# Kernel optimization log

Hardware: AMD Instinct MI355X
Metric: run time of the kernel (lower is better)

The kernel has to match this reference:

```python
import jax, jax.numpy as jnp
import numpy as np

B = 512
D = 64   # input feature dim
K = 63   # bilinear output dim (64 after the ones column)


def setup_inputs() -> dict:
    key = jax.random.key(0)
    ks = jax.random.split(key, 9)
    s = 1.0 / np.sqrt(D)  # torch Bilinear init scale (uniform bound); normal*s is fine for a baseline
    return {
        "x": jax.random.normal(ks[0], (B, D), jnp.float32),
        "y": jax.random.normal(ks[1], (B, D), jnp.float32),
        "z": jax.random.normal(ks[2], (B, D), jnp.float32),
        "W1": jax.random.normal(ks[3], (K, D, D), jnp.float32) * s,
        "b1": jax.random.normal(ks[4], (K,), jnp.float32) * s,
        "W2": jax.random.normal(ks[5], (K, D, D), jnp.float32) * s,
        "b2": jax.random.normal(ks[6], (K,), jnp.float32) * s,
        "W3": jax.random.normal(ks[7], (K, D, D), jnp.float32) * s,
        "b3": jax.random.normal(ks[8], (K,), jnp.float32) * s,
    }


def _bilinear(a, b, W, bias):
    # torch.nn.Bilinear: out[b,k] = sum_ij a[b,i] * W[k,i,j] * b[b,j] + bias[k]
    return jnp.einsum("bi,kij,bj->bk", a, W, b) + bias


def _append_ones(o):
    ones = jnp.ones((o.shape[0], 1), dtype=o.dtype)
    return jnp.concatenate([o, ones], axis=1)  # [B, 64]


def reference(x, y, z, W1, b1, W2, b2, W3, b3):
    o1 = _append_ones(_bilinear(x, y, W1, b1))  # [B,64]
    o2 = _append_ones(_bilinear(x, z, W2, b2))  # [B,64]
    o3 = _append_ones(_bilinear(y, z, W3, b3))  # [B,64]
    # bmm(o1[:,:,None], o2[:,None,:]).flatten then outer with o3 again:
    # index ordering is ((i*64 + j)*64 + k), matching bijk reshape.
    o123 = jnp.einsum("bi,bj,bk->bijk", o1, o2, o3)
    return o123.reshape(o123.shape[0], -1)  # [B, 262144]
```

## Files before the change

### kernel.cpp

```cpp
#include <hip/hip_runtime.h>
#include <hip/hip_bf16.h>

#define BATCH 512
#define DIM 64
#define KOUT 63

typedef float vf4 __attribute__((ext_vector_type(4)));

__global__ __launch_bounds__(256) void bilinear_kernel(
    const float* __restrict__ x, const float* __restrict__ y, const float* __restrict__ z,
    const float* __restrict__ W1, const float* __restrict__ b1,
    const float* __restrict__ W2, const float* __restrict__ b2,
    const float* __restrict__ W3, const float* __restrict__ b3,
    float* __restrict__ o ) {
    const int which = blockIdx.x >> 6;
    const int k     = blockIdx.x & 63;
    const int b     = blockIdx.y * 256 + threadIdx.x;

    float* outp = o + which * (BATCH * DIM);

    if (k == KOUT) {
        outp[b * DIM + KOUT] = 1.0f;
        return;
    }

    const float* A  = (which == 2) ? y : x;
    const float* C  = (which == 0) ? y : z;
    const float* W  = ((which == 0) ? W1 : (which == 1) ? W2 : W3) + k * (DIM * DIM);
    const float  bias = ((which == 0) ? b1 : (which == 1) ? b2 : b3)[k];

    __shared__ float sW[DIM * DIM];
    {
        const float4* W4  = (const float4*)W;
        float4*       sW4 = (float4*)sW;
        #pragma unroll
        for (int t = threadIdx.x; t < DIM * DIM / 4; t += 256) sW4[t] = W4[t];
    }
    __syncthreads();

    float c[DIM];
    {
        const float4* C4 = (const float4*)(C + b * DIM);
        #pragma unroll
        for (int q = 0; q < DIM / 4; q++) {
            float4 v = C4[q];
            c[4 * q + 0] = v.x; c[4 * q + 1] = v.y; c[4 * q + 2] = v.z; c[4 * q + 3] = v.w;
        }
    }

    const float* arow = A + b * DIM;
    const float4* sW4 = (const float4*)sW;
    float acc = bias;
    #pragma unroll 4
    for (int i = 0; i < DIM; i++) {
        float t = 0.0f;
        #pragma unroll
        for (int q = 0; q < DIM / 4; q++) {
            float4 w = sW4[i * (DIM / 4) + q];
            t = fmaf(w.x, c[4 * q + 0], t);
            t = fmaf(w.y, c[4 * q + 1], t);
            t = fmaf(w.z, c[4 * q + 2], t);
            t = fmaf(w.w, c[4 * q + 3], t);
        }
        acc = fmaf(arow[i], t, acc);
    }
    outp[b * DIM + k] = acc;
}

__global__ __launch_bounds__(256) void outer_kernel(
    const float* __restrict__ o , float* __restrict__ out) {
    const int b = blockIdx.x;
    __shared__ float s1[DIM];
    __shared__ float s2[DIM];
    __shared__ float s3f[DIM];

    const int t = threadIdx.x;
    if (t < 64)        s1[t]        = o[b * DIM + t];
    else if (t < 128)  s2[t - 64]   = o[BATCH * DIM + b * DIM + (t - 64)];
    else if (t < 192)  s3f[t - 128] = o[2 * BATCH * DIM + b * DIM + (t - 128)];
    __syncthreads();

    const vf4* s3 = (const vf4*)s3f;
    vf4* out4 = (vf4*)out + (size_t)b * 65536;

    #pragma unroll 4
    for (int f4 = t; f4 < 65536; f4 += 256) {
        const int k4 = f4 & 15;
        const int j  = (f4 >> 4) & 63;
        const int i  = f4 >> 10;
        const float s = s1[i] * s2[j];
        vf4 v = s3[k4] * s;
        __builtin_nontemporal_store(v, &out4[f4]);
    }
}

extern "C" void kernel_launch(void* const* d_in, const int* in_sizes, int n_in,
                              void* d_out, int out_size, void* d_ws, size_t ws_size,
                              hipStream_t stream) {
    const float* x  = (const float*)d_in[0];
    const float* y  = (const float*)d_in[1];
    const float* z  = (const float*)d_in[2];
    const float* W1 = (const float*)d_in[3];
    const float* b1 = (const float*)d_in[4];
    const float* W2 = (const float*)d_in[5];
    const float* b2 = (const float*)d_in[6];
    const float* W3 = (const float*)d_in[7];
    const float* b3 = (const float*)d_in[8];
    float* out = (float*)d_out;
    float* o   = (float*)d_ws;

    bilinear_kernel<<<dim3(192, 2), 256, 0, stream>>>(x, y, z, W1, b1, W2, b2, W3, b3, o);
    outer_kernel<<<dim3(BATCH), 256, 0, stream>>>(o, out);
}
```

Before: 568.3 us.

## Split outer-product kernel across 16 segments per batch row with precomputed scales

The outer kernel now launches 16 blocks per batch row, each writing a 4096-vector slice (four i values), instead of one block writing all 65536 vectors. Each thread precomputes its 16 s1*s2 products in registers and issues 16 fully unrolled nontemporal stores with no per-iteration index arithmetic or shared-memory reads. This raises the number of blocks in flight for the store-bound phase and removes the address and LDS work. In exchange, each block redundantly reloads the s2 and s3 rows, and every block pays its own launch and sync overhead.

```diff
diff --git a/kernel.cpp b/kernel.cpp
--- a/kernel.cpp
+++ b/kernel.cpp
@@ -1,5 +1,4 @@
 #include <hip/hip_runtime.h>
-#include <hip/hip_bf16.h>
 
 #define BATCH 512
 #define DIM 64
@@ -69,28 +68,35 @@
 
 __global__ __launch_bounds__(256) void outer_kernel(
     const float* __restrict__ o , float* __restrict__ out) {
-    const int b = blockIdx.x;
-    __shared__ float s1[DIM];
+    const int b   = blockIdx.x;
+    const int seg = blockIdx.y;
+
+    __shared__ float s1[4];
     __shared__ float s2[DIM];
     __shared__ float s3f[DIM];
 
     const int t = threadIdx.x;
-    if (t < 64)        s1[t]        = o[b * DIM + t];
-    else if (t < 128)  s2[t - 64]   = o[BATCH * DIM + b * DIM + (t - 64)];
-    else if (t < 192)  s3f[t - 128] = o[2 * BATCH * DIM + b * DIM + (t - 128)];
+    if (t < 64)        s2[t]        = o[BATCH * DIM + b * DIM + t];
+    else if (t < 128)  s3f[t - 64]  = o[2 * BATCH * DIM + b * DIM + (t - 64)];
+    else if (t < 132)  s1[t - 128]  = o[b * DIM + seg * 4 + (t - 128)];
     __syncthreads();
 
-    const vf4* s3 = (const vf4*)s3f;
-    vf4* out4 = (vf4*)out + (size_t)b * 65536;
+    const vf4 v3 = ((const vf4*)s3f)[t & 15];
+    const int jb = t >> 4;
 
-    #pragma unroll 4
-    for (int f4 = t; f4 < 65536; f4 += 256) {
-        const int k4 = f4 & 15;
-        const int j  = (f4 >> 4) & 63;
-        const int i  = f4 >> 10;
-        const float s = s1[i] * s2[j];
-        vf4 v = s3[k4] * s;
-        __builtin_nontemporal_store(v, &out4[f4]);
+    float p[4][4];
+    #pragma unroll
+    for (int ii = 0; ii < 4; ++ii) {
+        const float a = s1[ii];
+        #pragma unroll
+        for (int jc = 0; jc < 4; ++jc) p[ii][jc] = a * s2[jb + 16 * jc];
+    }
+
+    vf4* out4 = (vf4*)out + (size_t)b * 65536 + seg * 4096 + t;
+    #pragma unroll
+    for (int it = 0; it < 16; ++it) {
+        vf4 v = v3 * p[it >> 2][it & 3];
+        __builtin_nontemporal_store(v, &out4[it * 256]);
     }
 }
 
@@ -110,5 +116,5 @@
     float* o   = (float*)d_ws;
 
     bilinear_kernel<<<dim3(192, 2), 256, 0, stream>>>(x, y, z, W1, b1, W2, b2, W3, b3, o);
-    outer_kernel<<<dim3(BATCH), 256, 0, stream>>>(o, out);
+    outer_kernel<<<dim3(BATCH, 16), 256, 0, stream>>>(o, out);
 }
```

New measurement: 570.8 us. About the same (+0.4%).
